# Kernel optimization log

Hardware: AMD Instinct MI355X
Metric: run time of the kernel (lower is better)

Reference implementation:

```python
import jax, jax.numpy as jnp
import numpy as np
from functools import partial

# ---- module hyperparameters (from init_kwargs) ----
INP_DIM = 128
OUT_DIM = 128
NOISE_LEVEL = 0.1
AB_MVM = 8   # activation bits after MVM
IB = 8       # input activation bits
WB = 8       # weight bits
BATCH = 262144


def step_d(bits):
    return 2.0 ** (bits - 1)


def pact_a(x, a):
    # PACT clip: sign(x) * 0.5 * (|x| - ||x| - a| + a)
    return jnp.sign(x) * 0.5 * (jnp.abs(x) - jnp.abs(jnp.abs(x) - a) + a)


@partial(jax.custom_vjp, nondiff_argnums=(2,))
def quant_ste(x, x_range, bits):
    # fake-quantize x to `bits` bits over [-x_range, x_range], straight-through grad
    sd = step_d(bits)
    x01 = jnp.clip(x / x_range, -1.0 + 1.0 / sd, 1.0 - 1.0 / sd)
    return jnp.round(x01 * sd) / sd * x_range


def _quant_fwd(x, x_range, bits):
    return quant_ste(x, x_range, bits), x_range


def _quant_bwd(bits, x_range, g):
    # torch QuantFunc.backward: grad passes straight through to x, None for range
    return (g, jnp.zeros_like(x_range))


quant_ste.defvjp(_quant_fwd, _quant_bwd)


def _noisy_mm(x, w, b):
    # simulated analog MVM: quantized weights + per-tensor Gaussian noise
    k1, k2 = jax.random.split(jax.random.key(1234))
    noise_w = jax.random.normal(k1, w.shape, w.dtype) * w.max() * NOISE_LEVEL
    noise_b = jax.random.normal(k2, b.shape, b.dtype) * b.max() * NOISE_LEVEL
    wq = quant_ste(w, 1.0, WB)
    bq = quant_ste(b, 1.0, WB)
    return x @ (wq + noise_w) + bq + noise_b


custom_mm = jax.custom_vjp(_noisy_mm)


def _mm_fwd(x, w, b):
    return _noisy_mm(x, w, b), (x, w)


def _mm_bwd(res, g):
    # torch CustomMM.backward uses CLEAN (un-noised, un-quantized) weight/input
    x, w = res
    return (g @ w.T, x.T @ g, g.sum(0))


custom_mm.defvjp(_mm_fwd, _mm_bwd)


def setup_inputs() -> dict:
    key = jax.random.key(0)
    kx, kw = jax.random.split(key)
    x = jax.random.normal(kx, (BATCH, INP_DIM), dtype=jnp.float32)
    # weight init: uniform(-limit, limit) with limit = max(sqrt(6/inp_dim), 1.5/2^(wb-1))
    limit = max(np.sqrt(6.0 / INP_DIM), 1.5 / (2.0 ** (WB - 1)))
    weights = jax.random.uniform(kw, (INP_DIM, OUT_DIM), dtype=jnp.float32,
                                 minval=-limit, maxval=limit)
    bias = jnp.zeros((OUT_DIM,), dtype=jnp.float32)  # torch init: uniform(0, 0)
    a1 = jnp.array([4.0], dtype=jnp.float32)
    a2 = jnp.array([16.0], dtype=jnp.float32)
    return {"x": x, "weights": weights, "bias": bias, "a1": a1, "a2": a2}


def reference(x, weights, bias, a1, a2):
    # quant_pass(pact_a(CustomMM(quant_pass(pact_a(x,a1), ib, a1), W, b, nl, wb), a2), abMVM, a2)
    xq = quant_ste(pact_a(x, a1), a1, IB)          # [B, inp_dim]
    h = custom_mm(xq, weights, bias)               # [B, out_dim]
    return quant_ste(pact_a(h, a2), a2, AB_MVM)    # [B, out_dim]
```

## Files before the change

kernel.cpp:

```cpp
#include <hip/hip_runtime.h>
#include <stdint.h>

#define INP 128
#define OUTD 128
#define WT_STRIDE 136
#define THREEFRY_PARTITIONABLE 1

typedef __bf16 bf16x8 __attribute__((ext_vector_type(8)));
typedef float  floatx4 __attribute__((ext_vector_type(4)));

__device__ __forceinline__ uint32_t rotl32(uint32_t v, uint32_t n) {
  return (v << n) | (v >> (32u - n));
}
__device__ __forceinline__ void tf_round(uint32_t& x0, uint32_t& x1, uint32_t r) {
  x0 += x1; x1 = rotl32(x1, r); x1 ^= x0;
}
__device__ void threefry2x32(uint32_t k0, uint32_t k1, uint32_t c0, uint32_t c1,
                             uint32_t& o0, uint32_t& o1) {
  uint32_t k2 = k0 ^ k1 ^ 0x1BD11BDAu;
  uint32_t x0 = c0 + k0, x1 = c1 + k1;
  tf_round(x0,x1,13); tf_round(x0,x1,15); tf_round(x0,x1,26); tf_round(x0,x1,6);
  x0 += k1; x1 += k2 + 1u;
  tf_round(x0,x1,17); tf_round(x0,x1,29); tf_round(x0,x1,16); tf_round(x0,x1,24);
  x0 += k2; x1 += k0 + 2u;
  tf_round(x0,x1,13); tf_round(x0,x1,15); tf_round(x0,x1,26); tf_round(x0,x1,6);
  x0 += k0; x1 += k1 + 3u;
  tf_round(x0,x1,17); tf_round(x0,x1,29); tf_round(x0,x1,16); tf_round(x0,x1,24);
  x0 += k1; x1 += k2 + 4u;
  tf_round(x0,x1,13); tf_round(x0,x1,15); tf_round(x0,x1,26); tf_round(x0,x1,6);
  x0 += k2; x1 += k0 + 5u;
  o0 = x0; o1 = x1;
}

__device__ float erfinv_giles(float x) {
  float w = -logf((1.0f - x) * (1.0f + x));
  float p;
  if (w < 5.0f) {
    w = w - 2.5f;
    p = 2.81022636e-08f;
    p = fmaf(p, w, 3.43273939e-07f);
    p = fmaf(p, w, -3.5233877e-06f);
    p = fmaf(p, w, -4.39150654e-06f);
    p = fmaf(p, w, 0.00021858087f);
    p = fmaf(p, w, -0.00125372503f);
    p = fmaf(p, w, -0.00417768164f);
    p = fmaf(p, w, 0.246640727f);
    p = fmaf(p, w, 1.50140941f);
  } else {
    w = sqrtf(w) - 3.0f;
    p = -0.000200214257f;
    p = fmaf(p, w, 0.000100950558f);
    p = fmaf(p, w, 0.00134934322f);
    p = fmaf(p, w, -0.00367342844f);
    p = fmaf(p, w, 0.00573950773f);
    p = fmaf(p, w, -0.0076224613f);
    p = fmaf(p, w, 0.00943887047f);
    p = fmaf(p, w, 1.00167406f);
    p = fmaf(p, w, 2.83297682f);
  }
  return p * x;
}

__device__ float normal_from_bits(uint32_t bits) {
  const float lo = -0.999999940395355224609375f;
  uint32_t fb = (bits >> 9) | 0x3F800000u;
  float f = __uint_as_float(fb) - 1.0f;
  float u = fmaxf(lo, f * 2.0f + lo);
  return 1.41421356237309515f * erfinv_giles(u);
}

__device__ __forceinline__ uint32_t rand_bits(uint32_t ka, uint32_t kb, int i, int half) {
#if THREEFRY_PARTITIONABLE
  (void)half;
  uint32_t o0, o1;
  threefry2x32(ka, kb, 0u, (uint32_t)i, o0, o1);
  return o0 ^ o1;
#else
  uint32_t c0 = (i < half) ? (uint32_t)i : (uint32_t)(i - half);
  uint32_t o0, o1;
  threefry2x32(ka, kb, c0, c0 + (uint32_t)half, o0, o1);
  return (i < half) ? o0 : o1;
#endif
}

__global__ __launch_bounds__(256) void setup_reduce(
    const float* __restrict__ w, const float* __restrict__ bias,
    float* __restrict__ biasEff, float* __restrict__ scalars) {
  __shared__ float red[8];
  const int tid = threadIdx.x;

  float m = -3.4e38f;
  for (int i = tid; i < INP * OUTD; i += 256) m = fmaxf(m, w[i]);
  #pragma unroll
  for (int off = 1; off < 64; off <<= 1) m = fmaxf(m, __shfl_xor(m, off));
  float bm = (tid < OUTD) ? bias[tid] : -3.4e38f;
  #pragma unroll
  for (int off = 1; off < 64; off <<= 1) bm = fmaxf(bm, __shfl_xor(bm, off));
  if ((tid & 63) == 0) { red[tid >> 6] = m; red[4 + (tid >> 6)] = bm; }
  __syncthreads();
  const float wmax = fmaxf(fmaxf(red[0], red[1]), fmaxf(red[2], red[3]));
  const float bmax = fmaxf(fmaxf(red[4], red[5]), fmaxf(red[6], red[7]));
  if (tid == 0) { scalars[0] = wmax; scalars[1] = bmax; }

  uint32_t k2a, k2b;
#if THREEFRY_PARTITIONABLE
  threefry2x32(0u, 1234u, 0u, 1u, k2a, k2b);
#else
  { uint32_t a0, b0, a1, b1;
    threefry2x32(0u, 1234u, 0u, 2u, a0, b0);
    threefry2x32(0u, 1234u, 1u, 3u, a1, b1);
    k2a = b0; k2b = b1; }
#endif
  if (tid < OUTD) {
    float nrm = normal_from_bits(rand_bits(k2a, k2b, tid, OUTD / 2));
    float bv = bias[tid];
    float bq = rintf(fminf(fmaxf(bv * 128.f, -127.f), 127.f)) * 0.0078125f;
    biasEff[tid] = bq + (nrm * bmax) * 0.1f;
  }
}

__global__ __launch_bounds__(256) void setup_noise(
    const float* __restrict__ w, __bf16* __restrict__ wt,
    const float* __restrict__ scalars) {
  const int i = blockIdx.x * 256 + threadIdx.x;
  const float wmax = scalars[0];

  uint32_t k1a, k1b;
#if THREEFRY_PARTITIONABLE
  threefry2x32(0u, 1234u, 0u, 0u, k1a, k1b);
#else
  { uint32_t a0, b0, a1, b1;
    threefry2x32(0u, 1234u, 0u, 2u, a0, b0);
    threefry2x32(0u, 1234u, 1u, 3u, a1, b1);
    k1a = a0; k1b = a1; }
#endif

  float nrm = normal_from_bits(rand_bits(k1a, k1b, i, (INP * OUTD) / 2));
  int r = i >> 7, c = i & 127;
  float wv = w[i];
  float wq = rintf(fminf(fmaxf(wv * 128.f, -127.f), 127.f)) * 0.0078125f;
  wt[c * WT_STRIDE + r] = (__bf16)(wq + (nrm * wmax) * 0.1f);
}

__device__ __forceinline__ bf16x8 quant_a(const float* p, float s1, float r1) {
  floatx4 v0 = *(const floatx4*)p;
  floatx4 v1 = *(const floatx4*)(p + 4);
  bf16x8 a;
  #pragma unroll
  for (int i = 0; i < 4; ++i) {
    a[i]     = (__bf16)(rintf(fminf(fmaxf(v0[i] * s1, -127.f), 127.f)) * r1);
    a[i + 4] = (__bf16)(rintf(fminf(fmaxf(v1[i] * s1, -127.f), 127.f)) * r1);
  }
  return a;
}

__global__ __launch_bounds__(256) void linlayer_main(
    const float* __restrict__ x, const __bf16* __restrict__ wt,
    const float* __restrict__ biasEff, const float* __restrict__ a1p,
    const float* __restrict__ a2p, float* __restrict__ out, int nTiles) {
  __shared__ __attribute__((aligned(16))) __bf16 sW[OUTD * WT_STRIDE];
  __shared__ float sBias[OUTD];

  const int tid = threadIdx.x;

  {
    const uint4* src = (const uint4*)wt;
    uint4* dst = (uint4*)sW;
    for (int i = tid; i < (OUTD * WT_STRIDE * 2) / 16; i += 256) dst[i] = src[i];
  }
  if (tid < OUTD) sBias[tid] = biasEff[tid];

  const float a1 = a1p[0], a2 = a2p[0];
  const float s1 = 128.0f / a1, r1 = a1 * 0.0078125f;
  const float s2 = 128.0f / a2, r2 = a2 * 0.0078125f;

  __syncthreads();

  const int wave = tid >> 6;
  const int lane = tid & 63;
  const int n16  = lane & 15;
  const int quad = lane >> 4;

  for (int tile = blockIdx.x; tile < nTiles; tile += gridDim.x) {
    const long rowBase = (long)tile * 128 + wave * 32;

    floatx4 acc[2][8];
    #pragma unroll
    for (int rt = 0; rt < 2; ++rt)
      #pragma unroll
      for (int ct = 0; ct < 8; ++ct) acc[rt][ct] = (floatx4)0.0f;

    const float* xp0 = x + (size_t)(rowBase + n16) * INP + quad * 8;
    const float* xp1 = xp0 + (size_t)16 * INP;

    #pragma unroll
    for (int kc = 0; kc < 4; ++kc) {
      bf16x8 afrag0 = quant_a(xp0 + kc * 32, s1, r1);
      bf16x8 afrag1 = quant_a(xp1 + kc * 32, s1, r1);
      const int kOff = kc * 32 + quad * 8;
      #pragma unroll
      for (int ct = 0; ct < 8; ++ct) {
        bf16x8 wfrag = *(const bf16x8*)&sW[(ct * 16 + n16) * WT_STRIDE + kOff];
        acc[0][ct] = __builtin_amdgcn_mfma_f32_16x16x32_bf16(wfrag, afrag0, acc[0][ct], 0, 0, 0);
        acc[1][ct] = __builtin_amdgcn_mfma_f32_16x16x32_bf16(wfrag, afrag1, acc[1][ct], 0, 0, 0);
      }
    }

    #pragma unroll
    for (int rt = 0; rt < 2; ++rt) {
      const size_t row = (size_t)(rowBase + rt * 16 + n16);
      float* orow = out + row * OUTD;
      #pragma unroll
      for (int ct = 0; ct < 8; ++ct) {
        const int colBase = ct * 16 + quad * 4;
        floatx4 v;
        #pragma unroll
        for (int r = 0; r < 4; ++r) {
          float h = acc[rt][ct][r] + sBias[colBase + r];
          float t = fminf(fmaxf(h * s2, -127.0f), 127.0f);
          v[r] = rintf(t) * r2;
        }
        *(floatx4*)(orow + colBase) = v;
      }
    }
  }
}

extern "C" void kernel_launch(void* const* d_in, const int* in_sizes, int n_in,
                              void* d_out, int out_size, void* d_ws, size_t ws_size,
                              hipStream_t stream) {
  const float* x    = (const float*)d_in[0];
  const float* w    = (const float*)d_in[1];
  const float* bias = (const float*)d_in[2];
  const float* a1   = (const float*)d_in[3];
  const float* a2   = (const float*)d_in[4];
  float* out = (float*)d_out;

  __bf16* wt     = (__bf16*)d_ws;
  float* biasEff = (float*)((char*)d_ws + OUTD * WT_STRIDE * 2);
  float* scalars = (float*)((char*)d_ws + OUTD * WT_STRIDE * 2 + 512);

  const int rows   = in_sizes[0] / INP;
  const int nTiles = rows / 128;
  const int grid   = 1024;

  setup_reduce<<<1, 256, 0, stream>>>(w, bias, biasEff, scalars);
  setup_noise<<<64, 256, 0, stream>>>(w, wt, scalars);
  linlayer_main<<<grid, 256, 0, stream>>>(x, wt, biasEff, a1, a2, out, nTiles);
}
```

Baseline: 272.5 us.

## Double-buffer per-wave 16-row tiles with register prefetch of next x tile

Each wave now independently processes 16-row tiles instead of the block sharing 128-row tiles, and the next tile's x values are loaded into registers while the current tile is quantized, multiplied and stored. The prefetch of the first tile is issued before the shared-memory weight copy. The aim is to hide global-load latency behind MFMA and epilogue work in this bandwidth-bound kernel. In exchange it uses more registers per wave and drops the reuse of each weight fragment read across two row tiles, so LDS traffic per MFMA doubles.

```diff
diff --git a/kernel.cpp b/kernel.cpp
--- a/kernel.cpp
+++ b/kernel.cpp
@@ -142,9 +142,17 @@
   wt[c * WT_STRIDE + r] = (__bf16)(wq + (nrm * wmax) * 0.1f);
 }
 
-__device__ __forceinline__ bf16x8 quant_a(const float* p, float s1, float r1) {
-  floatx4 v0 = *(const floatx4*)p;
-  floatx4 v1 = *(const floatx4*)(p + 4);
+__device__ __forceinline__ void load_tile(floatx4 v[8], const float* __restrict__ x,
+                                          long tile, int n16, int quad) {
+  const float* p = x + ((size_t)(tile * 16 + n16) << 7) + quad * 8;
+  #pragma unroll
+  for (int kc = 0; kc < 4; ++kc) {
+    v[2 * kc]     = *(const floatx4*)(p + kc * 32);
+    v[2 * kc + 1] = *(const floatx4*)(p + kc * 32 + 4);
+  }
+}
+
+__device__ __forceinline__ bf16x8 quant_pair(floatx4 v0, floatx4 v1, float s1, float r1) {
   bf16x8 a;
   #pragma unroll
   for (int i = 0; i < 4; ++i) {
@@ -152,6 +160,40 @@
     a[i + 4] = (__bf16)(rintf(fminf(fmaxf(v1[i] * s1, -127.f), 127.f)) * r1);
   }
   return a;
+}
+
+__device__ __forceinline__ void compute_tile(
+    const floatx4 v[8], const __bf16* sW, const float* sBias,
+    float* __restrict__ out, long tile, int n16, int quad,
+    float s1, float r1, float s2, float r2) {
+  floatx4 acc[8];
+  #pragma unroll
+  for (int ct = 0; ct < 8; ++ct) acc[ct] = (floatx4)0.0f;
+
+  #pragma unroll
+  for (int kc = 0; kc < 4; ++kc) {
+    bf16x8 a = quant_pair(v[2 * kc], v[2 * kc + 1], s1, r1);
+    const int kOff = kc * 32 + quad * 8;
+    #pragma unroll
+    for (int ct = 0; ct < 8; ++ct) {
+      bf16x8 wfrag = *(const bf16x8*)&sW[(ct * 16 + n16) * WT_STRIDE + kOff];
+      acc[ct] = __builtin_amdgcn_mfma_f32_16x16x32_bf16(wfrag, a, acc[ct], 0, 0, 0);
+    }
+  }
+
+  float* orow = out + ((size_t)(tile * 16 + n16) << 7);
+  #pragma unroll
+  for (int ct = 0; ct < 8; ++ct) {
+    const int colBase = ct * 16 + quad * 4;
+    floatx4 o;
+    #pragma unroll
+    for (int r = 0; r < 4; ++r) {
+      float h = acc[ct][r] + sBias[colBase + r];
+      float t = fminf(fmaxf(h * s2, -127.0f), 127.0f);
+      o[r] = rintf(t) * r2;
+    }
+    *(floatx4*)(orow + colBase) = o;
+  }
 }
 
 __global__ __launch_bounds__(256) void linlayer_main(
@@ -161,7 +203,18 @@
   __shared__ __attribute__((aligned(16))) __bf16 sW[OUTD * WT_STRIDE];
   __shared__ float sBias[OUTD];
 
-  const int tid = threadIdx.x;
+  const int tid  = threadIdx.x;
+  const int lane = tid & 63;
+  const int n16  = lane & 15;
+  const int quad = lane >> 4;
+
+  const int nWaves = gridDim.x * 4;
+  const int waveId = blockIdx.x * 4 + (tid >> 6);
+  const long last  = nTiles - 1;
+
+  floatx4 bufA[8], bufB[8];
+  long t = waveId;
+  load_tile(bufA, x, (t <= last) ? t : last, n16, quad);
 
   {
     const uint4* src = (const uint4*)wt;
@@ -176,53 +229,17 @@
 
   __syncthreads();
 
-  const int wave = tid >> 6;
-  const int lane = tid & 63;
-  const int n16  = lane & 15;
-  const int quad = lane >> 4;
-
-  for (int tile = blockIdx.x; tile < nTiles; tile += gridDim.x) {
-    const long rowBase = (long)tile * 128 + wave * 32;
-
-    floatx4 acc[2][8];
-    #pragma unroll
-    for (int rt = 0; rt < 2; ++rt)
-      #pragma unroll
-      for (int ct = 0; ct < 8; ++ct) acc[rt][ct] = (floatx4)0.0f;
-
-    const float* xp0 = x + (size_t)(rowBase + n16) * INP + quad * 8;
-    const float* xp1 = xp0 + (size_t)16 * INP;
-
-    #pragma unroll
-    for (int kc = 0; kc < 4; ++kc) {
-      bf16x8 afrag0 = quant_a(xp0 + kc * 32, s1, r1);
-      bf16x8 afrag1 = quant_a(xp1 + kc * 32, s1, r1);
-      const int kOff = kc * 32 + quad * 8;
-      #pragma unroll
-      for (int ct = 0; ct < 8; ++ct) {
-        bf16x8 wfrag = *(const bf16x8*)&sW[(ct * 16 + n16) * WT_STRIDE + kOff];
-        acc[0][ct] = __builtin_amdgcn_mfma_f32_16x16x32_bf16(wfrag, afrag0, acc[0][ct], 0, 0, 0);
-        acc[1][ct] = __builtin_amdgcn_mfma_f32_16x16x32_bf16(wfrag, afrag1, acc[1][ct], 0, 0, 0);
-      }
-    }
-
-    #pragma unroll
-    for (int rt = 0; rt < 2; ++rt) {
-      const size_t row = (size_t)(rowBase + rt * 16 + n16);
-      float* orow = out + row * OUTD;
-      #pragma unroll
-      for (int ct = 0; ct < 8; ++ct) {
-        const int colBase = ct * 16 + quad * 4;
-        floatx4 v;
-        #pragma unroll
-        for (int r = 0; r < 4; ++r) {
-          float h = acc[rt][ct][r] + sBias[colBase + r];
-          float t = fminf(fmaxf(h * s2, -127.0f), 127.0f);
-          v[r] = rintf(t) * r2;
-        }
-        *(floatx4*)(orow + colBase) = v;
-      }
-    }
+  while (t <= last) {
+    long tn = t + nWaves;
+    load_tile(bufB, x, (tn <= last) ? tn : last, n16, quad);
+    compute_tile(bufA, sW, sBias, out, t, n16, quad, s1, r1, s2, r2);
+    t = tn;
+    if (t > last) break;
+
+    tn = t + nWaves;
+    load_tile(bufA, x, (tn <= last) ? tn : last, n16, quad);
+    compute_tile(bufB, sW, sBias, out, t, n16, quad, s1, r1, s2, r2);
+    t = tn;
   }
 }
 
@@ -241,7 +258,7 @@
   float* scalars = (float*)((char*)d_ws + OUTD * WT_STRIDE * 2 + 512);
 
   const int rows   = in_sizes[0] / INP;
-  const int nTiles = rows / 128;
+  const int nTiles = rows / 16;
   const int grid   = 1024;
 
   setup_reduce<<<1, 256, 0, stream>>>(w, bias, biasEff, scalars);
```

Result: no change. 270.9 us (median of 2 runs) (-0.6%).
